# Performance work log

Hardware: AMD Instinct MI355X
Metric: run time of the kernel (lower is better)

The kernel has to match this reference:

```python
import jax, jax.numpy as jnp
import numpy as np

KERNEL_SIZE = 5
SIGMA = 1.0
DARK_KS = 15


def _gaussian_kernel():
    x = jnp.arange(KERNEL_SIZE, dtype=jnp.float32) - KERNEL_SIZE // 2
    phi = jnp.exp(-0.5 * x * x / (SIGMA ** 2))
    phi = phi / (phi.sum() + 0.001)
    k2d = jnp.outer(phi, phi)                       # [5,5]
    return jnp.tile(k2d[None, None], (3, 1, 1, 1))  # [3,1,5,5] OIHW depthwise


def _tanh01(v):
    return jnp.tanh(v) * 0.5 + 0.5


def setup_inputs() -> dict:
    key = jax.random.key(0)
    k1, k2, k3 = jax.random.split(key, 3)
    # keep x strictly positive so x**param has well-defined gradients
    x = jax.random.uniform(k1, (16, 3, 512, 512), dtype=jnp.float32, minval=0.01, maxval=1.0)
    output1 = jax.random.normal(k2, (16, 7), dtype=jnp.float32)
    output2 = jax.random.normal(k3, (16, 4), dtype=jnp.float32)
    return {"x": x, "output1": output1, "output2": output2}


def reference(x, output1, output2):
    N, C, H, W = x.shape

    # ---- parameter squashing (clip_range + softmax weights) ----
    o1 = jnp.concatenate([
        _tanh01(output1[:, 0:1]) * 0.25 + 1.0,   # gamma param in [1, 1.25]
        _tanh01(output1[:, 1:2]) * 0.9 + 0.1,    # contrast alpha (dead branch)
        _tanh01(output1[:, 2:3]) * 2.0,          # sharpen lamda in [0, 2]
        _tanh01(output1[:, 3:4]),                # dehaze w in [0, 1]
        _tanh01(output1[:, 4:7]) * 0.1 + 0.95,   # WB gains in [0.95, 1.05]
    ], axis=1)
    o2 = jax.nn.softmax(_tanh01(output2), axis=1)  # [N,4] branch weights

    param = o1[:, 0][:, None, None, None]
    lamda = o1[:, 2][:, None, None, None]
    w = o1[:, 3][:, None, None, None]
    wb_params = o1[:, 4:7][:, :, None, None]

    # ---- WB ----
    x1 = jnp.clip(x * wb_params, 0.0, 1.0)

    # ---- GAMMA ----
    x2 = jnp.clip(x ** param + 0.001, 0.0, 1.0)

    # ---- SHARPEN (depthwise 5x5 gaussian blur, unsharp mask) ----
    gk = _gaussian_kernel()
    blur = jax.lax.conv_general_dilated(
        x, gk, window_strides=(1, 1), padding=((2, 2), (2, 2)),
        feature_group_count=3,
        dimension_numbers=("NCHW", "OIHW", "NCHW"))
    blur = jnp.clip(blur, 0.0, 1.0)
    x4 = jnp.clip(x + lamda * (x - blur), 0.0, 1.0)

    # ---- DEHAZE ----
    minc = jnp.min(x, axis=1, keepdims=True)  # [N,1,H,W]
    # avg_pool2d k=15 s=1 p=7 with count_include_pad=True -> sum window / 225
    dark = jax.lax.reduce_window(
        minc, 0.0, jax.lax.add, (1, 1, DARK_KS, DARK_KS), (1, 1, 1, 1),
        padding=[(0, 0), (0, 0), (DARK_KS // 2, DARK_KS // 2), (DARK_KS // 2, DARK_KS // 2)]
    ) / float(DARK_KS * DARK_KS)
    top_k = int(H * W * 0.05)
    flat_dark = dark.reshape(N, -1)
    _, top_idx = jax.lax.top_k(flat_dark, top_k)            # [N, top_k]
    flat_img = x.reshape(N, C, -1)
    sel = jnp.take_along_axis(flat_img, top_idx[:, None, :], axis=2)  # [N,C,top_k]
    A = sel.mean(axis=2)[:, :, None, None]                  # atmospheric light
    trans = 1.0 - w * dark
    trans = jnp.where(trans > 0.1, trans, jnp.float32(0.1))
    x5 = jnp.clip((x - A) / (trans + 0.001) + A, 0.0, 1.0)

    # ---- weighted combination (contrast branch is computed but unused upstream) ----
    w0 = o2[:, 0][:, None, None, None]
    w1 = o2[:, 1][:, None, None, None]
    w2 = o2[:, 2][:, None, None, None]
    w3 = o2[:, 3][:, None, None, None]
    x_sum = x + 0.1 * (w0 * x1 + w1 * x2 + w2 * x4 + w3 * x5)
    x_sum = x_sum / (jnp.sum(o2, axis=1)[:, None, None, None] + 0.001)

    # ---- per-sample per-channel min-max normalization ----
    min_vals = jnp.min(x_sum, axis=(2, 3), keepdims=True)
    max_vals = jnp.max(x_sum, axis=(2, 3), keepdims=True)
    return (x_sum - min_vals) / (max_vals - min_vals + 1e-07)
```

## Files before the change

### kernel.cpp

```cpp
#include <hip/hip_runtime.h>
#include <math.h>

#define NS   16
#define HH   512
#define WW   512
#define HW   (HH*WW)
#define TOPK 13107
#define NBIN 1024

#define O_O1   0
#define O_O2   112
#define O_DEN  176
#define O_KN   304
#define O_MMP  512
#define O_PART 25088
#define O_DARK 33280


#define G0 0.054466787f
#define G1 0.244103071f
#define G2 0.402457854f

__device__ __forceinline__ float tanh01(float v) { return tanhf(v)*0.5f + 0.5f; }
__device__ __forceinline__ float clamp01(float v) { return fminf(fmaxf(v, 0.0f), 1.0f); }
__device__ __forceinline__ int dark_bin(float v) {
  int b = (int)(v * (float)NBIN);
  return b > (NBIN-1) ? (NBIN-1) : (b < 0 ? 0 : b);
}

__global__ void k_zero(unsigned* __restrict__ hist) {
  int i = blockIdx.x * 256 + threadIdx.x;
  uint4 z; z.x = 0u; z.y = 0u; z.z = 0u; z.w = 0u;
  ((uint4*)hist)[i] = z;
}

__global__ void __launch_bounds__(512)
k_dark(const float* __restrict__ x, float* __restrict__ wsf, unsigned* __restrict__ hist) {
  __shared__ __align__(16) float sm[6240 + 78*64];
  float* minc = sm;
  unsigned* lh = (unsigned*)sm;
  float* hsum = sm + 6240;
  int tid = threadIdx.x;
  int w0 = blockIdx.x * 64, h0 = blockIdx.y * 64, n = blockIdx.z;
  const float* xb = x + (size_t)n*3*HW;

  bool interior = (w0 >= 8) && (w0 + 72 <= WW) && (h0 >= 7) && (h0 + 71 <= HH);
  if (interior) {
    for (int i = tid; i < 78*20; i += 512) {
      int r = i / 20, q = i - r*20;
      size_t o = (size_t)(h0 - 7 + r)*WW + (w0 - 8 + 4*q);
      float4 a = *(const float4*)&xb[o];
      float4 b = *(const float4*)&xb[HW + o];
      float4 c = *(const float4*)&xb[2*HW + o];
      float4 v;
      v.x = fminf(fminf(a.x,b.x),c.x); v.y = fminf(fminf(a.y,b.y),c.y);
      v.z = fminf(fminf(a.z,b.z),c.z); v.w = fminf(fminf(a.w,b.w),c.w);
      *(float4*)&minc[r*80 + 4*q] = v;
    }
  } else {
    for (int i = tid; i < 78*20; i += 512) {
      int r = i / 20, q = i - r*20;
      int hm = h0 - 7 + r, wc = w0 - 8 + 4*q;
      float4 v; v.x = 0.f; v.y = 0.f; v.z = 0.f; v.w = 0.f;
      if (hm >= 0 && hm < HH && wc >= 0 && wc < WW) {
        size_t o = (size_t)hm*WW + wc;
        float4 a = *(const float4*)&xb[o];
        float4 b = *(const float4*)&xb[HW + o];
        float4 c = *(const float4*)&xb[2*HW + o];
        v.x = fminf(fminf(a.x,b.x),c.x); v.y = fminf(fminf(a.y,b.y),c.y);
        v.z = fminf(fminf(a.z,b.z),c.z); v.w = fminf(fminf(a.w,b.w),c.w);
      }
      *(float4*)&minc[r*80 + 4*q] = v;
    }
  }
  __syncthreads();
  for (int i = tid; i < 78*16; i += 512) {
    int r = i >> 4, c4 = (i & 15) * 4;
    const float4* mr = (const float4*)&minc[r*80];
    int qb = c4 >> 2;
    float m[20];
    #pragma unroll
    for (int t = 0; t < 5; ++t) {
      float4 v = mr[qb + t];
      m[4*t] = v.x; m[4*t+1] = v.y; m[4*t+2] = v.z; m[4*t+3] = v.w;
    }
    float s = 0.f;
    #pragma unroll
    for (int j = 1; j <= 15; ++j) s += m[j];
    float4 o;
    o.x = s; s += m[16] - m[1];
    o.y = s; s += m[17] - m[2];
    o.z = s; s += m[18] - m[3];
    o.w = s;
    *(float4*)&hsum[r*64 + c4] = o;
  }
  __syncthreads();
  for (int i = tid; i < NBIN*4; i += 512) lh[i] = 0u;
  __syncthreads();
  {
    int c = tid & 63, ty = tid >> 6, r0 = ty * 8;
    int rep = tid & 3;
    float s = 0.f;
    #pragma unroll
    for (int j = 0; j < 15; ++j) s += hsum[(r0 + j)*64 + c];
    float* dk = wsf + O_DARK + (size_t)n*HW;
    int prevb = -1; unsigned cnt = 0;
    #pragma unroll
    for (int i = 0; i < 8; ++i) {
      int r = r0 + i;
      float v = s * (1.0f/225.0f);
      dk[(size_t)(h0 + r)*WW + w0 + c] = v;
      int b = dark_bin(v);
      if (b == prevb) { cnt++; }
      else {
        if (cnt) atomicAdd(&lh[(prevb << 2) | rep], cnt);
        prevb = b; cnt = 1u;
      }
      if (i < 7) s += hsum[(r + 15)*64 + c] - hsum[r*64 + c];
    }
    atomicAdd(&lh[(prevb << 2) | rep], cnt);
  }
  __syncthreads();
  unsigned* gh = hist + n*NBIN;
  for (int b = tid; b < NBIN; b += 512) {
    unsigned v = lh[4*b] + lh[4*b+1] + lh[4*b+2] + lh[4*b+3];
    if (v) atomicAdd(&gh[b], v);
  }
}

__global__ void __launch_bounds__(256)
k_asum(const float* __restrict__ x, float* __restrict__ wsf,
       const unsigned* __restrict__ hist, unsigned* __restrict__ wsu,
       const float* __restrict__ o1, const float* __restrict__ o2) {
  __shared__ __align__(16) unsigned lh[NBIN];
  __shared__ unsigned spp[256];
  __shared__ int sh_bsel;
  __shared__ float bl[4][7];
  int tid = threadIdx.x;
  int n = blockIdx.x >> 6, chunk = blockIdx.x & 63;
  {
    uint4 v = ((const uint4*)(hist + n*NBIN))[tid];
    *(uint4*)&lh[tid*4] = v;
    spp[tid] = v.x + v.y + v.z + v.w;
  }
  __syncthreads();
  if (tid == 0) {
    const unsigned K = TOPK;
    unsigned cum = 0; int bsel = 0;
    for (int t = 255; t >= 0; --t) {
      if (cum + spp[t] >= K) {
        bsel = t*4;
        for (int b = t*4 + 3; b >= t*4; --b) {
          if (cum + lh[b] >= K) { bsel = b; break; }
          cum += lh[b];
        }
        break;
      }
      cum += spp[t];
    }
    sh_bsel = bsel;
    if (chunk == 0) {
      wsu[O_KN + n] = K - cum;
      wsf[O_O1+n*7+0] = tanh01(o1[n*7+0])*0.25f + 1.0f;
      wsf[O_O1+n*7+1] = tanh01(o1[n*7+1])*0.9f  + 0.1f;
      wsf[O_O1+n*7+2] = tanh01(o1[n*7+2])*2.0f;
      wsf[O_O1+n*7+3] = tanh01(o1[n*7+3]);
      wsf[O_O1+n*7+4] = tanh01(o1[n*7+4])*0.1f + 0.95f;
      wsf[O_O1+n*7+5] = tanh01(o1[n*7+5])*0.1f + 0.95f;
      wsf[O_O1+n*7+6] = tanh01(o1[n*7+6])*0.1f + 0.95f;
      float q0 = expf(tanh01(o2[n*4+0]));
      float q1 = expf(tanh01(o2[n*4+1]));
      float q2 = expf(tanh01(o2[n*4+2]));
      float q3 = expf(tanh01(o2[n*4+3]));
      float s = q0+q1+q2+q3;
      q0 /= s; q1 /= s; q2 /= s; q3 /= s;
      wsf[O_O2+n*4+0]=q0; wsf[O_O2+n*4+1]=q1; wsf[O_O2+n*4+2]=q2; wsf[O_O2+n*4+3]=q3;
      wsf[O_DEN+n] = (q0+q1+q2+q3) + 0.001f;
    }
  }
  __syncthreads();
  int bsel = sh_bsel;
  const float4* db = (const float4*)(wsf + O_DARK + (size_t)n*HW + (size_t)chunk*4096);
  const float4* x0 = (const float4*)(x + (size_t)n*3*HW + (size_t)chunk*4096);
  const float4* x1 = x0 + HW/4;
  const float4* x2 = x0 + HW/2;
  float s0=0,s1=0,s2=0,e0=0,e1=0,e2=0,ec=0;
  #pragma unroll
  for (int k = 0; k < 4; ++k) {
    int idx = k*256 + tid;
    float4 d = db[idx];
    int bbx = dark_bin(d.x), bby = dark_bin(d.y);
    int bbz = dark_bin(d.z), bbw = dark_bin(d.w);
    int bmax = bbx > bby ? bbx : bby;
    bmax = bbz > bmax ? bbz : bmax;
    bmax = bbw > bmax ? bbw : bmax;
    if (bmax >= bsel) {
      float4 a = x0[idx], b = x1[idx], c = x2[idx];
      #define ACC(BB, AX, BX, CX) { \
        bool gt = (BB > bsel), eq = (BB == bsel); \
        s0 += gt ? AX : 0.f; s1 += gt ? BX : 0.f; s2 += gt ? CX : 0.f; \
        e0 += eq ? AX : 0.f; e1 += eq ? BX : 0.f; e2 += eq ? CX : 0.f; \
        ec += eq ? 1.f : 0.f; }
      ACC(bbx, a.x, b.x, c.x) ACC(bby, a.y, b.y, c.y)
      ACC(bbz, a.z, b.z, c.z) ACC(bbw, a.w, b.w, c.w)
      #undef ACC
    }
  }
  #pragma unroll
  for (int off = 32; off; off >>= 1) {
    s0 += __shfl_down(s0, off); s1 += __shfl_down(s1, off); s2 += __shfl_down(s2, off);
    e0 += __shfl_down(e0, off); e1 += __shfl_down(e1, off); e2 += __shfl_down(e2, off);
    ec += __shfl_down(ec, off);
  }
  int wave = tid >> 6, lane = tid & 63;
  if (lane == 0) {
    bl[wave][0]=s0; bl[wave][1]=s1; bl[wave][2]=s2;
    bl[wave][3]=e0; bl[wave][4]=e1; bl[wave][5]=e2; bl[wave][6]=ec;
  }
  __syncthreads();
  if (tid < 7) wsf[O_PART + blockIdx.x*8 + tid] =
      bl[0][tid] + bl[1][tid] + bl[2][tid] + bl[3][tid];
}

__global__ void __launch_bounds__(256)
k_main(const float* __restrict__ x, float* __restrict__ wsf,
       const unsigned* __restrict__ wsu, float* __restrict__ out) {
  __shared__ __align__(16) float xs[20*72];
  __shared__ __align__(16) float hb[20*64];
  __shared__ float rmn[4], rmx[4];
  __shared__ float shA[3];
  int tid = threadIdx.x;
  int w0 = blockIdx.x * 64, h0 = blockIdx.y * 16, n = blockIdx.z;
  int r = tid >> 4, c4 = (tid & 15) * 4;
  int wave = tid >> 6, lane = tid & 63;
  int bxy = blockIdx.y * 8 + blockIdx.x;
  float4 dk = *(const float4*)&wsf[O_DARK + (size_t)n*HW + (size_t)(h0+r)*WW + w0 + c4];
  float param = wsf[O_O1 + n*7 + 0];
  float lamda = wsf[O_O1 + n*7 + 2];
  float wpar  = wsf[O_O1 + n*7 + 3];
  float q0 = wsf[O_O2 + n*4 + 0], q1 = wsf[O_O2 + n*4 + 1];
  float q2 = wsf[O_O2 + n*4 + 2], q3 = wsf[O_O2 + n*4 + 3];
  float rden = 1.0f / wsf[O_DEN + n];
  bool interior = (w0 >= 4) && (w0 + 68 <= WW) && (h0 >= 2) && (h0 + 18 <= HH);
  if (tid < 64) {
    const float* p = wsf + O_PART + (size_t)(n*64 + tid)*8;
    float s0=p[0], s1=p[1], s2=p[2], e0=p[3], e1=p[4], e2=p[5], ec=p[6];
    #pragma unroll
    for (int off = 32; off; off >>= 1) {
      s0 += __shfl_down(s0, off); s1 += __shfl_down(s1, off); s2 += __shfl_down(s2, off);
      e0 += __shfl_down(e0, off); e1 += __shfl_down(e1, off); e2 += __shfl_down(e2, off);
      ec += __shfl_down(ec, off);
    }
    if (tid == 0) {
      float kn = (float)wsu[O_KN + n];
      float ce = fmaxf(ec, 1.0f);
      shA[0] = (s0 + kn * (e0 / ce)) * (1.0f/(float)TOPK);
      shA[1] = (s1 + kn * (e1 / ce)) * (1.0f/(float)TOPK);
      shA[2] = (s2 + kn * (e2 / ce)) * (1.0f/(float)TOPK);
    }
  }

  for (int c = 0; c < 3; ++c) {
    int z = n*3 + c;
    const float* xc = x + (size_t)z*HW;
    if (interior) {
      for (int i = tid; i < 360; i += 256) {
        int rr = i / 18, q = i - rr*18;
        *(float4*)&xs[rr*72 + 4*q] =
            *(const float4*)&xc[(size_t)(h0 - 2 + rr)*WW + (w0 - 4 + 4*q)];
      }
    } else {
      for (int i = tid; i < 360; i += 256) {
        int rr = i / 18, q = i - rr*18;
        int gh = h0 - 2 + rr, gw = w0 - 4 + 4*q;
        float4 v; v.x = 0.f; v.y = 0.f; v.z = 0.f; v.w = 0.f;
        if (gh >= 0 && gh < HH && gw >= 0 && gw < WW)
          v = *(const float4*)&xc[(size_t)gh*WW + gw];
        *(float4*)&xs[rr*72 + 4*q] = v;
      }
    }
    __syncthreads();
    for (int i = tid; i < 320; i += 256) {
      int rr = i >> 4, cc4 = (i & 15) * 4;
      const float4* xr = (const float4*)&xs[rr*72];
      int qb = cc4 >> 2;
      float4 A4 = xr[qb], B4 = xr[qb+1], C4 = xr[qb+2];
      float m2=A4.z, m3=A4.w, m4=B4.x, m5=B4.y, m6=B4.z, m7=B4.w, m8=C4.x, m9=C4.y;
      float4 o;
      o.x = G0*(m2+m6) + G1*(m3+m5) + G2*m4;
      o.y = G0*(m3+m7) + G1*(m4+m6) + G2*m5;
      o.z = G0*(m4+m8) + G1*(m5+m7) + G2*m6;
      o.w = G0*(m5+m9) + G1*(m6+m8) + G2*m7;
      *(float4*)&hb[rr*64 + cc4] = o;
    }
    __syncthreads();
    float wb = wsf[O_O1 + n*7 + 4 + c];
    float A  = shA[c];
    float4 xv = *(const float4*)&xs[(r+2)*72 + c4 + 4];
    float4 b0 = *(const float4*)&hb[(r+0)*64 + c4];
    float4 b1 = *(const float4*)&hb[(r+1)*64 + c4];
    float4 b2 = *(const float4*)&hb[(r+2)*64 + c4];
    float4 b3 = *(const float4*)&hb[(r+3)*64 + c4];
    float4 b4 = *(const float4*)&hb[(r+4)*64 + c4];
    float4 osum;
    float mnv = 3.4e38f, mxv = -3.4e38f;
    #define PIX(OX, XV, B0, B1, B2, B3, B4, DK) { \
      float blur = clamp01(G0*(B0+B4) + G1*(B1+B3) + G2*B2); \
      float x4v = clamp01(XV + lamda*(XV - blur)); \
      float x1v = clamp01(XV * wb); \
      float x2v = clamp01(__expf(param*__logf(XV)) + 0.001f); \
      float tr = 1.0f - wpar*DK; tr = tr > 0.1f ? tr : 0.1f; \
      float x5v = clamp01((XV - A) * __builtin_amdgcn_rcpf(tr + 0.001f) + A); \
      OX = (XV + 0.1f*(q0*x1v + q1*x2v + q2*x4v + q3*x5v)) * rden; \
      mnv = fminf(mnv, OX); mxv = fmaxf(mxv, OX); }
    PIX(osum.x, xv.x, b0.x, b1.x, b2.x, b3.x, b4.x, dk.x)
    PIX(osum.y, xv.y, b0.y, b1.y, b2.y, b3.y, b4.y, dk.y)
    PIX(osum.z, xv.z, b0.z, b1.z, b2.z, b3.z, b4.z, dk.z)
    PIX(osum.w, xv.w, b0.w, b1.w, b2.w, b3.w, b4.w, dk.w)
    #undef PIX
    *(float4*)&out[(size_t)z*HW + (size_t)(h0+r)*WW + w0 + c4] = osum;
    #pragma unroll
    for (int off = 32; off; off >>= 1) {
      mnv = fminf(mnv, __shfl_down(mnv, off));
      mxv = fmaxf(mxv, __shfl_down(mxv, off));
    }
    if (lane == 0) { rmn[wave] = mnv; rmx[wave] = mxv; }
    __syncthreads();
    if (tid == 0) {
      mnv = fminf(fminf(rmn[0], rmn[1]), fminf(rmn[2], rmn[3]));
      mxv = fmaxf(fmaxf(rmx[0], rmx[1]), fmaxf(rmx[2], rmx[3]));
      wsf[O_MMP + z*512 + bxy]       = mnv;
      wsf[O_MMP + z*512 + 256 + bxy] = mxv;
    }
  }
}

__global__ void __launch_bounds__(256)
k_norm(float* __restrict__ out, const float* __restrict__ wsf) {
  __shared__ float rmn[4], rmx[4];
  int tid = threadIdx.x;
  int nc = blockIdx.x >> 5;
  int sub = blockIdx.x & 31;
  float mn = wsf[O_MMP + nc*512 + tid];
  float mx = wsf[O_MMP + nc*512 + 256 + tid];
  #pragma unroll
  for (int off = 32; off; off >>= 1) {
    mn = fminf(mn, __shfl_down(mn, off));
    mx = fmaxf(mx, __shfl_down(mx, off));
  }
  int wave = tid >> 6, lane = tid & 63;
  if (lane == 0) { rmn[wave] = mn; rmx[wave] = mx; }
  __syncthreads();
  mn = fminf(fminf(rmn[0], rmn[1]), fminf(rmn[2], rmn[3]));
  mx = fmaxf(fmaxf(rmx[0], rmx[1]), fmaxf(rmx[2], rmx[3]));
  float sc = 1.0f / (mx - mn + 1e-7f);
  float4* o4 = (float4*)out + (size_t)nc*65536 + (size_t)sub*2048;
  #pragma unroll
  for (int k = 0; k < 8; ++k) {
    float4 v = o4[k*256 + tid];
    v.x = (v.x - mn) * sc; v.y = (v.y - mn) * sc;
    v.z = (v.z - mn) * sc; v.w = (v.w - mn) * sc;
    o4[k*256 + tid] = v;
  }
}

extern "C" void kernel_launch(void* const* d_in, const int* in_sizes, int n_in,
                              void* d_out, int out_size, void* d_ws, size_t ws_size,
                              hipStream_t stream) {
  const float* x  = (const float*)d_in[0];
  const float* o1 = (const float*)d_in[1];
  const float* o2 = (const float*)d_in[2];
  float* out = (float*)d_out;
  float* wsf = (float*)d_ws;
  unsigned* wsu = (unsigned*)d_ws;
  unsigned* hist = (unsigned*)(out + (size_t)16*HW);

  k_zero<<<dim3(16), dim3(256), 0, stream>>>(hist);
  k_dark<<<dim3(8, 8, 16), dim3(512), 0, stream>>>(x, wsf, hist);
  k_asum<<<dim3(1024), dim3(256), 0, stream>>>(x, wsf, hist, wsu, o1, o2);
  k_main<<<dim3(8, 32, 16), dim3(256), 0, stream>>>(x, wsf, wsu, out);
  k_norm<<<dim3(1536), dim3(256), 0, stream>>>(out, wsf);
}
```

Before: 170.2 us.

## Double rows per thread in main kernel, parallelize top-k bin search, hoist param squashing

The main fused kernel now gives each thread two output rows (a 32-row tile per block), so halo loads and horizontal blur work are amortized over more outputs, and the blur buffer row pitch is padded to 68. The serial single-thread histogram scan in k_asum is replaced by a wave-level suffix scan that finds the threshold bin in parallel. Parameter squashing moves into k_zero. The trade is more shared memory and registers per block, half as many blocks in k_main, and k_norm now reducing only 128 partial min/max entries.

```diff
diff --git a/kernel.cpp b/kernel.cpp
--- a/kernel.cpp
+++ b/kernel.cpp
@@ -28,10 +28,29 @@
   return b > (NBIN-1) ? (NBIN-1) : (b < 0 ? 0 : b);
 }
 
-__global__ void k_zero(unsigned* __restrict__ hist) {
+__global__ void k_zero(unsigned* __restrict__ hist, float* __restrict__ wsf,
+                       const float* __restrict__ o1, const float* __restrict__ o2) {
   int i = blockIdx.x * 256 + threadIdx.x;
   uint4 z; z.x = 0u; z.y = 0u; z.z = 0u; z.w = 0u;
   ((uint4*)hist)[i] = z;
+  if (threadIdx.x == 0) {
+    int n = blockIdx.x;
+    wsf[O_O1+n*7+0] = tanh01(o1[n*7+0])*0.25f + 1.0f;
+    wsf[O_O1+n*7+1] = tanh01(o1[n*7+1])*0.9f  + 0.1f;
+    wsf[O_O1+n*7+2] = tanh01(o1[n*7+2])*2.0f;
+    wsf[O_O1+n*7+3] = tanh01(o1[n*7+3]);
+    wsf[O_O1+n*7+4] = tanh01(o1[n*7+4])*0.1f + 0.95f;
+    wsf[O_O1+n*7+5] = tanh01(o1[n*7+5])*0.1f + 0.95f;
+    wsf[O_O1+n*7+6] = tanh01(o1[n*7+6])*0.1f + 0.95f;
+    float q0 = expf(tanh01(o2[n*4+0]));
+    float q1 = expf(tanh01(o2[n*4+1]));
+    float q2 = expf(tanh01(o2[n*4+2]));
+    float q3 = expf(tanh01(o2[n*4+3]));
+    float s = q0+q1+q2+q3;
+    q0 /= s; q1 /= s; q2 /= s; q3 /= s;
+    wsf[O_O2+n*4+0]=q0; wsf[O_O2+n*4+1]=q1; wsf[O_O2+n*4+2]=q2; wsf[O_O2+n*4+3]=q3;
+    wsf[O_DEN+n] = (q0+q1+q2+q3) + 0.001f;
+  }
 }
 
 __global__ void __launch_bounds__(512)
@@ -130,13 +149,15 @@
 
 __global__ void __launch_bounds__(256)
 k_asum(const float* __restrict__ x, float* __restrict__ wsf,
-       const unsigned* __restrict__ hist, unsigned* __restrict__ wsu,
-       const float* __restrict__ o1, const float* __restrict__ o2) {
+       const unsigned* __restrict__ hist, unsigned* __restrict__ wsu) {
   __shared__ __align__(16) unsigned lh[NBIN];
   __shared__ unsigned spp[256];
+  __shared__ unsigned wtot[4];
   __shared__ int sh_bsel;
+  __shared__ unsigned sh_kn;
   __shared__ float bl[4][7];
   int tid = threadIdx.x;
+  int lane = tid & 63, wave = tid >> 6;
   int n = blockIdx.x >> 6, chunk = blockIdx.x & 63;
   {
     uint4 v = ((const uint4*)(hist + n*NBIN))[tid];
@@ -144,42 +165,32 @@
     spp[tid] = v.x + v.y + v.z + v.w;
   }
   __syncthreads();
-  if (tid == 0) {
-    const unsigned K = TOPK;
-    unsigned cum = 0; int bsel = 0;
-    for (int t = 255; t >= 0; --t) {
-      if (cum + spp[t] >= K) {
-        bsel = t*4;
-        for (int b = t*4 + 3; b >= t*4; --b) {
-          if (cum + lh[b] >= K) { bsel = b; break; }
-          cum += lh[b];
-        }
-        break;
-      }
-      cum += spp[t];
+  unsigned sv = spp[tid];
+  #pragma unroll
+  for (int off = 1; off < 64; off <<= 1) {
+    unsigned u = __shfl_down(sv, off);
+    if (lane + off < 64) sv += u;
+  }
+  if (lane == 0) wtot[wave] = sv;
+  __syncthreads();
+  unsigned above = 0;
+  #pragma unroll
+  for (int w2 = 1; w2 < 4; ++w2) above += (wave + w2 < 4) ? wtot[wave + w2] : 0u;
+  unsigned S = sv + above;
+  unsigned Snext = S - spp[tid];
+  if (S >= (unsigned)TOPK && Snext < (unsigned)TOPK) {
+    unsigned cum = Snext;
+    int bsel = tid*4;
+    for (int b = tid*4 + 3; b >= tid*4; --b) {
+      if (cum + lh[b] >= (unsigned)TOPK) { bsel = b; break; }
+      cum += lh[b];
     }
     sh_bsel = bsel;
-    if (chunk == 0) {
-      wsu[O_KN + n] = K - cum;
-      wsf[O_O1+n*7+0] = tanh01(o1[n*7+0])*0.25f + 1.0f;
-      wsf[O_O1+n*7+1] = tanh01(o1[n*7+1])*0.9f  + 0.1f;
-      wsf[O_O1+n*7+2] = tanh01(o1[n*7+2])*2.0f;
-      wsf[O_O1+n*7+3] = tanh01(o1[n*7+3]);
-      wsf[O_O1+n*7+4] = tanh01(o1[n*7+4])*0.1f + 0.95f;
-      wsf[O_O1+n*7+5] = tanh01(o1[n*7+5])*0.1f + 0.95f;
-      wsf[O_O1+n*7+6] = tanh01(o1[n*7+6])*0.1f + 0.95f;
-      float q0 = expf(tanh01(o2[n*4+0]));
-      float q1 = expf(tanh01(o2[n*4+1]));
-      float q2 = expf(tanh01(o2[n*4+2]));
-      float q3 = expf(tanh01(o2[n*4+3]));
-      float s = q0+q1+q2+q3;
-      q0 /= s; q1 /= s; q2 /= s; q3 /= s;
-      wsf[O_O2+n*4+0]=q0; wsf[O_O2+n*4+1]=q1; wsf[O_O2+n*4+2]=q2; wsf[O_O2+n*4+3]=q3;
-      wsf[O_DEN+n] = (q0+q1+q2+q3) + 0.001f;
-    }
+    sh_kn = (unsigned)TOPK - cum;
   }
   __syncthreads();
   int bsel = sh_bsel;
+  if (tid == 0 && chunk == 0) wsu[O_KN + n] = sh_kn;
   const float4* db = (const float4*)(wsf + O_DARK + (size_t)n*HW + (size_t)chunk*4096);
   const float4* x0 = (const float4*)(x + (size_t)n*3*HW + (size_t)chunk*4096);
   const float4* x1 = x0 + HW/4;
@@ -212,7 +223,6 @@
     e0 += __shfl_down(e0, off); e1 += __shfl_down(e1, off); e2 += __shfl_down(e2, off);
     ec += __shfl_down(ec, off);
   }
-  int wave = tid >> 6, lane = tid & 63;
   if (lane == 0) {
     bl[wave][0]=s0; bl[wave][1]=s1; bl[wave][2]=s2;
     bl[wave][3]=e0; bl[wave][4]=e1; bl[wave][5]=e2; bl[wave][6]=ec;
@@ -225,23 +235,25 @@
 __global__ void __launch_bounds__(256)
 k_main(const float* __restrict__ x, float* __restrict__ wsf,
        const unsigned* __restrict__ wsu, float* __restrict__ out) {
-  __shared__ __align__(16) float xs[20*72];
-  __shared__ __align__(16) float hb[20*64];
+  __shared__ __align__(16) float xs[36*72];
+  __shared__ __align__(16) float hb[36*68];
   __shared__ float rmn[4], rmx[4];
   __shared__ float shA[3];
   int tid = threadIdx.x;
-  int w0 = blockIdx.x * 64, h0 = blockIdx.y * 16, n = blockIdx.z;
-  int r = tid >> 4, c4 = (tid & 15) * 4;
+  int w0 = blockIdx.x * 64, h0 = blockIdx.y * 32, n = blockIdx.z;
+  int r2 = tid >> 4, c4 = (tid & 15) * 4;
   int wave = tid >> 6, lane = tid & 63;
   int bxy = blockIdx.y * 8 + blockIdx.x;
-  float4 dk = *(const float4*)&wsf[O_DARK + (size_t)n*HW + (size_t)(h0+r)*WW + w0 + c4];
+  const float* dkp = wsf + O_DARK + (size_t)n*HW + (size_t)(h0 + 2*r2)*WW + w0 + c4;
+  float4 dk0 = *(const float4*)dkp;
+  float4 dk1 = *(const float4*)(dkp + WW);
   float param = wsf[O_O1 + n*7 + 0];
   float lamda = wsf[O_O1 + n*7 + 2];
   float wpar  = wsf[O_O1 + n*7 + 3];
   float q0 = wsf[O_O2 + n*4 + 0], q1 = wsf[O_O2 + n*4 + 1];
   float q2 = wsf[O_O2 + n*4 + 2], q3 = wsf[O_O2 + n*4 + 3];
   float rden = 1.0f / wsf[O_DEN + n];
-  bool interior = (w0 >= 4) && (w0 + 68 <= WW) && (h0 >= 2) && (h0 + 18 <= HH);
+  bool interior = (w0 >= 4) && (w0 + 68 <= WW) && (h0 >= 2) && (h0 + 34 <= HH);
   if (tid < 64) {
     const float* p = wsf + O_PART + (size_t)(n*64 + tid)*8;
     float s0=p[0], s1=p[1], s2=p[2], e0=p[3], e1=p[4], e2=p[5], ec=p[6];
@@ -264,13 +276,13 @@
     int z = n*3 + c;
     const float* xc = x + (size_t)z*HW;
     if (interior) {
-      for (int i = tid; i < 360; i += 256) {
+      for (int i = tid; i < 648; i += 256) {
         int rr = i / 18, q = i - rr*18;
         *(float4*)&xs[rr*72 + 4*q] =
             *(const float4*)&xc[(size_t)(h0 - 2 + rr)*WW + (w0 - 4 + 4*q)];
       }
     } else {
-      for (int i = tid; i < 360; i += 256) {
+      for (int i = tid; i < 648; i += 256) {
         int rr = i / 18, q = i - rr*18;
         int gh = h0 - 2 + rr, gw = w0 - 4 + 4*q;
         float4 v; v.x = 0.f; v.y = 0.f; v.z = 0.f; v.w = 0.f;
@@ -280,7 +292,7 @@
       }
     }
     __syncthreads();
-    for (int i = tid; i < 320; i += 256) {
+    for (int i = tid; i < 576; i += 256) {
       int rr = i >> 4, cc4 = (i & 15) * 4;
       const float4* xr = (const float4*)&xs[rr*72];
       int qb = cc4 >> 2;
@@ -291,18 +303,20 @@
       o.y = G0*(m3+m7) + G1*(m4+m6) + G2*m5;
       o.z = G0*(m4+m8) + G1*(m5+m7) + G2*m6;
       o.w = G0*(m5+m9) + G1*(m6+m8) + G2*m7;
-      *(float4*)&hb[rr*64 + cc4] = o;
+      *(float4*)&hb[rr*68 + cc4] = o;
     }
     __syncthreads();
     float wb = wsf[O_O1 + n*7 + 4 + c];
     float A  = shA[c];
-    float4 xv = *(const float4*)&xs[(r+2)*72 + c4 + 4];
-    float4 b0 = *(const float4*)&hb[(r+0)*64 + c4];
-    float4 b1 = *(const float4*)&hb[(r+1)*64 + c4];
-    float4 b2 = *(const float4*)&hb[(r+2)*64 + c4];
-    float4 b3 = *(const float4*)&hb[(r+3)*64 + c4];
-    float4 b4 = *(const float4*)&hb[(r+4)*64 + c4];
-    float4 osum;
+    float4 xv0 = *(const float4*)&xs[(2*r2+2)*72 + c4 + 4];
+    float4 xv1 = *(const float4*)&xs[(2*r2+3)*72 + c4 + 4];
+    float4 b0 = *(const float4*)&hb[(2*r2+0)*68 + c4];
+    float4 b1 = *(const float4*)&hb[(2*r2+1)*68 + c4];
+    float4 b2 = *(const float4*)&hb[(2*r2+2)*68 + c4];
+    float4 b3 = *(const float4*)&hb[(2*r2+3)*68 + c4];
+    float4 b4 = *(const float4*)&hb[(2*r2+4)*68 + c4];
+    float4 b5 = *(const float4*)&hb[(2*r2+5)*68 + c4];
+    float4 os0, os1;
     float mnv = 3.4e38f, mxv = -3.4e38f;
     #define PIX(OX, XV, B0, B1, B2, B3, B4, DK) { \
       float blur = clamp01(G0*(B0+B4) + G1*(B1+B3) + G2*B2); \
@@ -313,12 +327,18 @@
       float x5v = clamp01((XV - A) * __builtin_amdgcn_rcpf(tr + 0.001f) + A); \
       OX = (XV + 0.1f*(q0*x1v + q1*x2v + q2*x4v + q3*x5v)) * rden; \
       mnv = fminf(mnv, OX); mxv = fmaxf(mxv, OX); }
-    PIX(osum.x, xv.x, b0.x, b1.x, b2.x, b3.x, b4.x, dk.x)
-    PIX(osum.y, xv.y, b0.y, b1.y, b2.y, b3.y, b4.y, dk.y)
-    PIX(osum.z, xv.z, b0.z, b1.z, b2.z, b3.z, b4.z, dk.z)
-    PIX(osum.w, xv.w, b0.w, b1.w, b2.w, b3.w, b4.w, dk.w)
+    PIX(os0.x, xv0.x, b0.x, b1.x, b2.x, b3.x, b4.x, dk0.x)
+    PIX(os0.y, xv0.y, b0.y, b1.y, b2.y, b3.y, b4.y, dk0.y)
+    PIX(os0.z, xv0.z, b0.z, b1.z, b2.z, b3.z, b4.z, dk0.z)
+    PIX(os0.w, xv0.w, b0.w, b1.w, b2.w, b3.w, b4.w, dk0.w)
+    PIX(os1.x, xv1.x, b1.x, b2.x, b3.x, b4.x, b5.x, dk1.x)
+    PIX(os1.y, xv1.y, b1.y, b2.y, b3.y, b4.y, b5.y, dk1.y)
+    PIX(os1.z, xv1.z, b1.z, b2.z, b3.z, b4.z, b5.z, dk1.z)
+    PIX(os1.w, xv1.w, b1.w, b2.w, b3.w, b4.w, b5.w, dk1.w)
     #undef PIX
-    *(float4*)&out[(size_t)z*HW + (size_t)(h0+r)*WW + w0 + c4] = osum;
+    float* op = out + (size_t)z*HW + (size_t)(h0 + 2*r2)*WW + w0 + c4;
+    *(float4*)op = os0;
+    *(float4*)(op + WW) = os1;
     #pragma unroll
     for (int off = 32; off; off >>= 1) {
       mnv = fminf(mnv, __shfl_down(mnv, off));
@@ -341,8 +361,8 @@
   int tid = threadIdx.x;
   int nc = blockIdx.x >> 5;
   int sub = blockIdx.x & 31;
-  float mn = wsf[O_MMP + nc*512 + tid];
-  float mx = wsf[O_MMP + nc*512 + 256 + tid];
+  float mn = (tid < 128) ? wsf[O_MMP + nc*512 + tid]       :  3.4e38f;
+  float mx = (tid < 128) ? wsf[O_MMP + nc*512 + 256 + tid] : -3.4e38f;
   #pragma unroll
   for (int off = 32; off; off >>= 1) {
     mn = fminf(mn, __shfl_down(mn, off));
@@ -375,9 +395,9 @@
   unsigned* wsu = (unsigned*)d_ws;
   unsigned* hist = (unsigned*)(out + (size_t)16*HW);
 
-  k_zero<<<dim3(16), dim3(256), 0, stream>>>(hist);
+  k_zero<<<dim3(16), dim3(256), 0, stream>>>(hist, wsf, o1, o2);
   k_dark<<<dim3(8, 8, 16), dim3(512), 0, stream>>>(x, wsf, hist);
-  k_asum<<<dim3(1024), dim3(256), 0, stream>>>(x, wsf, hist, wsu, o1, o2);
-  k_main<<<dim3(8, 32, 16), dim3(256), 0, stream>>>(x, wsf, wsu, out);
+  k_asum<<<dim3(1024), dim3(256), 0, stream>>>(x, wsf, hist, wsu);
+  k_main<<<dim3(8, 16, 16), dim3(256), 0, stream>>>(x, wsf, wsu, out);
   k_norm<<<dim3(1536), dim3(256), 0, stream>>>(out, wsf);
 }
```

Measured after the change: 165.4 us. 2.8% less time.
